# Kernel optimization log

Measured on AMD Instinct MI355X. Metric: run time of the kernel, lower is better.

The kernel has to match this reference:

```python
import jax, jax.numpy as jnp
import numpy as np

N_NODES = 50000
N_EDGES = 800000
IN_DIM = 256
EMB_DIM = 256
N_COMS = 4
D_COM = EMB_DIM // N_COMS  # 64
BN_EPS = 1e-5


def setup_inputs() -> dict:
    key = jax.random.key(0)
    ks = jax.random.split(key, 16)
    s1 = 1.0 / np.sqrt(IN_DIM)
    s2 = 1.0 / np.sqrt(D_COM)
    return {
        "x": jax.random.normal(ks[0], (N_NODES, IN_DIM), jnp.float32),
        "edge_index": jax.random.randint(ks[1], (2, N_EDGES), 0, N_NODES, jnp.int32),
        "ew": jax.random.uniform(ks[2], (N_COMS, N_EDGES), jnp.float32),
        "W1_0": jax.random.normal(ks[3], (N_COMS, IN_DIM, D_COM), jnp.float32) * s1,
        "b1_0": jnp.zeros((N_COMS, D_COM), jnp.float32),
        "W2_0": jax.random.normal(ks[4], (N_COMS, D_COM, D_COM), jnp.float32) * s2,
        "b2_0": jnp.zeros((N_COMS, D_COM), jnp.float32),
        "g0": jnp.ones((N_COMS, D_COM), jnp.float32),
        "bt0": jnp.zeros((N_COMS, D_COM), jnp.float32),
        "W1_1": jax.random.normal(ks[5], (N_COMS, D_COM, D_COM), jnp.float32) * s2,
        "b1_1": jnp.zeros((N_COMS, D_COM), jnp.float32),
        "W2_1": jax.random.normal(ks[6], (N_COMS, D_COM, D_COM), jnp.float32) * s2,
        "b2_1": jnp.zeros((N_COMS, D_COM), jnp.float32),
        "g1": jnp.ones((N_COMS, D_COM), jnp.float32),
        "bt1": jnp.zeros((N_COMS, D_COM), jnp.float32),
        "encW": jax.random.normal(ks[7], (IN_DIM, EMB_DIM), jnp.float32) * s1,
        "encb": jnp.zeros((EMB_DIM,), jnp.float32),
    }


def _gin_bn_relu(h, src, dst, w, W1, b1, W2, b2, gamma, beta):
    # weighted scatter-add aggregation: agg[i] = sum_{e:(j->i)} w_e * h[j]
    msg = h[src] * w[:, None]                       # [E, F]
    agg = jax.ops.segment_sum(msg, dst, num_segments=N_NODES)
    z = h + agg                                      # eps = 0 (train_eps=False)
    z = jax.nn.relu(z @ W1 + b1) @ W2 + b2           # GIN MLP
    mu = jnp.mean(z, axis=0)
    var = jnp.var(z, axis=0)
    z = gamma * (z - mu) * jax.lax.rsqrt(var + BN_EPS) + beta
    return jax.nn.relu(z)                            # dropout: eval mode no-op


def reference(x, edge_index, ew, W1_0, b1_0, W2_0, b2_0, g0, bt0,
              W1_1, b1_1, W2_1, b2_1, g1, bt1, encW, encb):
    src, dst = edge_index[0], edge_index[1]
    outs1, outs2 = [], []
    for k in range(N_COMS):
        h1 = _gin_bn_relu(x, src, dst, ew[k], W1_0[k], b1_0[k], W2_0[k], b2_0[k], g0[k], bt0[k])
        h2 = _gin_bn_relu(h1, src, dst, ew[k], W1_1[k], b1_1[k], W2_1[k], b2_1[k], g1[k], bt1[k])
        outs1.append(h1)
        outs2.append(h2)
    out1 = jnp.concatenate(outs1, axis=-1)  # [N, emb_dim]
    out2 = jnp.concatenate(outs2, axis=-1)  # [N, emb_dim]
    enc = x @ encW + encb                   # input_encoder
    return (enc, out1, out2)
```

## Files before the change

kernel.cpp:

```cpp
#include <hip/hip_runtime.h>

#define NN 50000
#define NE 800000
#define FDIM 256
#define SCAN_BLOCKS 196
#define MMG 782
#define G32 1563

typedef __attribute__((ext_vector_type(8))) short short8v;
typedef __attribute__((ext_vector_type(4))) float float4v;

__device__ __forceinline__ unsigned short f2bf(float f) {
  unsigned u = __float_as_uint(f);
  unsigned r = (u + 0x7fffu + ((u >> 16) & 1u)) >> 16;
  return (unsigned short)r;
}
__device__ __forceinline__ float bf2f(unsigned short b) {
  return __uint_as_float(((unsigned)b) << 16);
}


__global__ __launch_bounds__(256) void k_hist(const int* __restrict__ dst, int* __restrict__ deg16,
                                              int* __restrict__ rank) {
  int e = blockIdx.x * 256 + threadIdx.x;
  if (e < NE) rank[e] = atomicAdd(&deg16[dst[e] << 4], 1);
}

__device__ __forceinline__ int block_incl_scan(int v, int* wsum) {
  const int tid = threadIdx.x;
  const int lane = tid & 63;
  const int w = tid >> 6;
  int incl = v;
  #pragma unroll
  for (int off = 1; off < 64; off <<= 1) {
    int tmp = __shfl_up(incl, off, 64);
    if (lane >= off) incl += tmp;
  }
  if (lane == 63) wsum[w] = incl;
  __syncthreads();
  int woff = 0;
  #pragma unroll
  for (int k = 0; k < 3; k++)
    if (k < w) woff += wsum[k];
  return woff + incl;
}

__global__ __launch_bounds__(256) void k_scan_a(const int* __restrict__ deg16, int* __restrict__ partial) {
  __shared__ int wsum[4];
  int i = blockIdx.x * 256 + threadIdx.x;
  int v = (i < NN) ? deg16[i << 4] : 0;
  int incl = block_incl_scan(v, wsum);
  if (threadIdx.x == 255) partial[blockIdx.x] = incl;
}

__global__ __launch_bounds__(256) void k_scanb_wprep(int* __restrict__ partial, int* __restrict__ offs,
                                                     const float* __restrict__ W1_0, const float* __restrict__ encW,
                                                     const float* __restrict__ W1_1, const float* __restrict__ W2_0,
                                                     const float* __restrict__ W2_1, unsigned short* __restrict__ Bt1,
                                                     unsigned short* __restrict__ BtE, unsigned short* __restrict__ Wb11,
                                                     unsigned short* __restrict__ Wb20, unsigned short* __restrict__ Wb21) {
  if (blockIdx.x == 256) {
    __shared__ int wsum[4];
    int tid = threadIdx.x;
    int v = (tid < SCAN_BLOCKS) ? partial[tid] : 0;
    int incl = block_incl_scan(v, wsum);
    if (tid < SCAN_BLOCKS) partial[tid] = incl - v;
    if (tid == 255) offs[NN] = incl;
    return;
  }
  const int t = blockIdx.x;
  const int k = threadIdx.x;
  const int c = t >> 6, j = t & 63;
  Bt1[t * 256 + k] = f2bf(W1_0[c * 16384 + k * 64 + j]);
  BtE[t * 256 + k] = f2bf(encW[k * 256 + t]);
  if (k < 64) {
    Wb11[c * 4096 + j * 64 + k] = f2bf(W1_1[c * 4096 + k * 64 + j]);
    Wb20[c * 4096 + j * 64 + k] = f2bf(W2_0[c * 4096 + k * 64 + j]);
    Wb21[c * 4096 + j * 64 + k] = f2bf(W2_1[c * 4096 + k * 64 + j]);
  }
}

__global__ __launch_bounds__(256) void k_scan_c(const int* __restrict__ deg16, const int* __restrict__ partial,
                                                int* __restrict__ offs) {
  __shared__ int wsum[4];
  int i = blockIdx.x * 256 + threadIdx.x;
  int v = (i < NN) ? deg16[i << 4] : 0;
  int incl = block_incl_scan(v, wsum);
  int excl = partial[blockIdx.x] + incl - v;
  if (i < NN) offs[i] = excl;
}

__global__ __launch_bounds__(256) void k_fill_mm(const float* __restrict__ x,
                                                 const unsigned short* __restrict__ Bt1,
                                                 const unsigned short* __restrict__ BtE,
                                                 const float* __restrict__ encb,
                                                 const int* __restrict__ srcA, const int* __restrict__ dstA,
                                                 const float* __restrict__ ew, const int* __restrict__ rank,
                                                 const int* __restrict__ offs,
                                                 int4* __restrict__ recs,
                                                 unsigned short* __restrict__ Pout,
                                                 float* __restrict__ encout) {
  __shared__ __align__(16) unsigned short xs[32][264];
  const int tid = threadIdx.x;
  const int lane = tid & 63;
  const int w = tid >> 6;
  const int isE = blockIdx.y;
  const int colw = w * 64;
  const int row0 = blockIdx.x * 32;
  const int lr = lane & 15;
  const int lk = (lane >> 4) * 8;
  const int rbase = (lane >> 4) * 4;

  const int e = (isE * G32 + blockIdx.x) * 256 + tid;
  const bool ev = e < NE;
  const int ec = ev ? e : 0;
  int sA = srcA[ec];
  int dA = dstA[ec];
  int rk = rank[ec];
  float w0 = ew[ec], w1 = ew[NE + ec], w2 = ew[2 * NE + ec], w3 = ew[3 * NE + ec];
  int ob = offs[dA];

  const unsigned short* Bt = isE ? BtE : Bt1;
  const unsigned short* Bptr[4];
  #pragma unroll
  for (int ct = 0; ct < 4; ct++) Bptr[ct] = Bt + (size_t)(colw + ct * 16 + lr) * 256 + lk;

  short8v bcur[4];
  #pragma unroll
  for (int ct = 0; ct < 4; ct++) bcur[ct] = *reinterpret_cast<const short8v*>(Bptr[ct]);

  float4 xv[8];
  #pragma unroll
  for (int it = 0; it < 8; it++) {
    int idx = it * 256 + tid;
    int grow = row0 + (idx >> 6);
    if (grow >= NN) grow = NN - 1;
    xv[it] = *reinterpret_cast<const float4*>(x + (size_t)grow * 256 + (idx & 63) * 4);
  }
  #pragma unroll
  for (int it = 0; it < 8; it++) {
    int idx = it * 256 + tid;
    ushort4 o;
    o.x = f2bf(xv[it].x); o.y = f2bf(xv[it].y); o.z = f2bf(xv[it].z); o.w = f2bf(xv[it].w);
    *reinterpret_cast<ushort4*>(&xs[idx >> 6][(idx & 63) * 4]) = o;
  }

  if (ev) {
    unsigned p01 = (unsigned)f2bf(w0) | ((unsigned)f2bf(w1) << 16);
    unsigned p23 = (unsigned)f2bf(w2) | ((unsigned)f2bf(w3) << 16);
    recs[ob + rk] = make_int4(sA, (int)p01, (int)p23, 0);
  }
  __syncthreads();

  float4v acc[2][4];
  #pragma unroll
  for (int rt = 0; rt < 2; rt++)
    #pragma unroll
    for (int ct = 0; ct < 4; ct++) acc[rt][ct] = (float4v){0.f, 0.f, 0.f, 0.f};

  #pragma unroll
  for (int ks8 = 0; ks8 < 8; ks8++) {
    const int ks = ks8 * 32;
    short8v bnxt[4];
    if (ks8 < 7) {
      #pragma unroll
      for (int ct = 0; ct < 4; ct++) bnxt[ct] = *reinterpret_cast<const short8v*>(Bptr[ct] + ks + 32);
    }
    short8v a[2];
    #pragma unroll
    for (int rt = 0; rt < 2; rt++)
      a[rt] = *reinterpret_cast<const short8v*>(&xs[rt * 16 + lr][ks + lk]);
    #pragma unroll
    for (int rt = 0; rt < 2; rt++)
      #pragma unroll
      for (int ct = 0; ct < 4; ct++)
        acc[rt][ct] = __builtin_amdgcn_mfma_f32_16x16x32_bf16(a[rt], bcur[ct], acc[rt][ct], 0, 0, 0);
    if (ks8 < 7) {
      #pragma unroll
      for (int ct = 0; ct < 4; ct++) bcur[ct] = bnxt[ct];
    }
  }

  __syncthreads();
  if (!isE) {
    #pragma unroll
    for (int rt = 0; rt < 2; rt++)
      #pragma unroll
      for (int ct = 0; ct < 4; ct++) {
        const int col = colw + ct * 16 + lr;
        #pragma unroll
        for (int r = 0; r < 4; r++) xs[rt * 16 + rbase + r][col] = f2bf(acc[rt][ct][r]);
      }
    __syncthreads();
    #pragma unroll
    for (int it = 0; it < 4; it++) {
      int idx = it * 256 + tid;
      int row = idx >> 5;
      int p = idx & 31;
      if (row0 + row < NN)
        *reinterpret_cast<short8v*>(Pout + (size_t)(row0 + row) * 256 + p * 8) =
            *reinterpret_cast<const short8v*>(&xs[row][p * 8]);
    }
  } else {
    float bv[4];
    #pragma unroll
    for (int ct = 0; ct < 4; ct++) bv[ct] = encb[colw + ct * 16 + lr];
    float (*cs)[132] = reinterpret_cast<float(*)[132]>(&xs[0][0]);
    #pragma unroll
    for (int ph = 0; ph < 2; ph++) {
      if ((colw >> 7) == ph) {
        #pragma unroll
        for (int rt = 0; rt < 2; rt++)
          #pragma unroll
          for (int ct = 0; ct < 4; ct++) {
            const int col = colw + ct * 16 + lr - ph * 128;
            #pragma unroll
            for (int r = 0; r < 4; r++) cs[rt * 16 + rbase + r][col] = acc[rt][ct][r] + bv[ct];
          }
      }
      __syncthreads();
      #pragma unroll
      for (int it = 0; it < 4; it++) {
        int idx = it * 256 + tid;
        int row = idx >> 5;
        int p = idx & 31;
        if (row0 + row < NN)
          *reinterpret_cast<float4*>(encout + (size_t)(row0 + row) * 256 + ph * 128 + p * 4) =
              *reinterpret_cast<const float4*>(&cs[row][p * 4]);
      }
      __syncthreads();
    }
  }
}

__global__ __launch_bounds__(256) void k_agg(const unsigned short* __restrict__ P,
                                             const int* __restrict__ offs, const int4* __restrict__ recs,
                                             const float* __restrict__ b1, unsigned short* __restrict__ Rb) {
  const int lane = threadIdx.x & 63;
  const int wid = threadIdx.x >> 6;
  const int i = blockIdx.x * 4 + wid;
  const int half = lane >> 5;
  const int l32 = lane & 31;
  const int col0 = l32 * 8;
  const int c = l32 >> 3;

  const int es = offs[i], ee = offs[i + 1];
  float acc[8];
  #pragma unroll
  for (int j = 0; j < 8; j++) acc[j] = 0.f;

  for (int base = es; base < ee; base += 16) {
    int sq[8];
    float wq[8];
    #pragma unroll
    for (int q = 0; q < 8; q++) {
      int e = base + 2 * q + half;
      bool valid = e < ee;
      int4 rv = recs[valid ? e : es];
      sq[q] = rv.x;
      unsigned p = (c < 2) ? (unsigned)rv.y : (unsigned)rv.z;
      unsigned short wb = (c & 1) ? (unsigned short)(p >> 16) : (unsigned short)(p & 0xffff);
      wq[q] = valid ? bf2f(wb) : 0.f;
    }
    short8v pq[8];
    #pragma unroll
    for (int q = 0; q < 8; q++)
      pq[q] = *reinterpret_cast<const short8v*>(P + (size_t)sq[q] * 256 + col0);
    #pragma unroll
    for (int q = 0; q < 8; q++)
      #pragma unroll
      for (int j = 0; j < 8; j++)
        acc[j] = fmaf(wq[q], bf2f((unsigned short)pq[q][j]), acc[j]);
  }

  #pragma unroll
  for (int j = 0; j < 8; j++) acc[j] += __shfl_xor(acc[j], 32);

  if (half == 0) {
    short8v ps = *reinterpret_cast<const short8v*>(P + (size_t)i * 256 + col0);
    float4 b4a = *reinterpret_cast<const float4*>(b1 + col0);
    float4 b4b = *reinterpret_cast<const float4*>(b1 + col0 + 4);
    float bb[8] = {b4a.x, b4a.y, b4a.z, b4a.w, b4b.x, b4b.y, b4b.z, b4b.w};
    short8v out;
    #pragma unroll
    for (int j = 0; j < 8; j++) {
      float r = bf2f((unsigned short)ps[j]) + acc[j] + bb[j];
      out[j] = (short)f2bf(r > 0.f ? r : 0.f);
    }
    *reinterpret_cast<short8v*>(Rb + (size_t)i * 256 + col0) = out;
  }
}

__global__ __launch_bounds__(256) void k_bd_stats(const unsigned short* __restrict__ A,
                                                  const unsigned short* __restrict__ Wz,
                                                  float* __restrict__ bnsum, float* __restrict__ bnsq) {
  const int lane = threadIdx.x & 63;
  const int c = threadIdx.x >> 6;
  const int row0 = blockIdx.x * 64;
  const int lr = lane & 15;
  const int lk = (lane >> 4) * 8;

  const unsigned short* Aptr[4];
  #pragma unroll
  for (int rt = 0; rt < 4; rt++) {
    int row = row0 + rt * 16 + lr;
    if (row >= NN) row = NN - 1;
    Aptr[rt] = A + (size_t)row * 256 + c * 64 + lk;
  }

  float4v acc[4][4];
  #pragma unroll
  for (int rt = 0; rt < 4; rt++)
    #pragma unroll
    for (int ct = 0; ct < 4; ct++) acc[rt][ct] = (float4v){0.f, 0.f, 0.f, 0.f};

  #pragma unroll
  for (int ks = 0; ks < 64; ks += 32) {
    short8v a[4], b[4];
    #pragma unroll
    for (int rt = 0; rt < 4; rt++) a[rt] = *reinterpret_cast<const short8v*>(Aptr[rt] + ks);
    #pragma unroll
    for (int ct = 0; ct < 4; ct++)
      b[ct] = *reinterpret_cast<const short8v*>(Wz + (size_t)c * 4096 + (ct * 16 + lr) * 64 + ks + lk);
    #pragma unroll
    for (int rt = 0; rt < 4; rt++)
      #pragma unroll
      for (int ct = 0; ct < 4; ct++)
        acc[rt][ct] = __builtin_amdgcn_mfma_f32_16x16x32_bf16(a[rt], b[ct], acc[rt][ct], 0, 0, 0);
  }

  #pragma unroll
  for (int ct = 0; ct < 4; ct++) {
    const int col = c * 64 + ct * 16 + lr;
    float s1 = 0.f, s2 = 0.f;
    #pragma unroll
    for (int rt = 0; rt < 4; rt++) {
      #pragma unroll
      for (int r = 0; r < 4; r++) {
        const int row = row0 + rt * 16 + (lane >> 4) * 4 + r;
        if (row < NN) {
          float v = acc[rt][ct][r];
          s1 += v;
          s2 += v * v;
        }
      }
    }
    s1 += __shfl_xor(s1, 16); s1 += __shfl_xor(s1, 32);
    s2 += __shfl_xor(s2, 16); s2 += __shfl_xor(s2, 32);
    if (lane < 16) {
      atomicAdd(&bnsum[col], s1);
      atomicAdd(&bnsq[col], s2);
    }
  }
}

template <int WITH_P2>
__global__ __launch_bounds__(256) void k_bd_bn(const unsigned short* __restrict__ A,
                                               const unsigned short* __restrict__ Wz,
                                               const float* __restrict__ bnsum, const float* __restrict__ bnsq,
                                               const float* __restrict__ g, const float* __restrict__ bt,
                                               const unsigned short* __restrict__ Wp,
                                               float* __restrict__ Hout, unsigned short* __restrict__ P2out) {
  __shared__ __align__(16) unsigned short h_lds[64][264];
  const int lane = threadIdx.x & 63;
  const int c = threadIdx.x >> 6;
  const int row0 = blockIdx.x * 64;
  const int lr = lane & 15;
  const int lk = (lane >> 4) * 8;
  const int rbase = (lane >> 4) * 4;

  const unsigned short* Aptr[4];
  #pragma unroll
  for (int rt = 0; rt < 4; rt++) {
    int row = row0 + rt * 16 + lr;
    if (row >= NN) row = NN - 1;
    Aptr[rt] = A + (size_t)row * 256 + c * 64 + lk;
  }

  float4v acc[4][4];
  #pragma unroll
  for (int rt = 0; rt < 4; rt++)
    #pragma unroll
    for (int ct = 0; ct < 4; ct++) acc[rt][ct] = (float4v){0.f, 0.f, 0.f, 0.f};

  #pragma unroll
  for (int ks = 0; ks < 64; ks += 32) {
    short8v a[4], b[4];
    #pragma unroll
    for (int rt = 0; rt < 4; rt++) a[rt] = *reinterpret_cast<const short8v*>(Aptr[rt] + ks);
    #pragma unroll
    for (int ct = 0; ct < 4; ct++)
      b[ct] = *reinterpret_cast<const short8v*>(Wz + (size_t)c * 4096 + (ct * 16 + lr) * 64 + ks + lk);
    #pragma unroll
    for (int rt = 0; rt < 4; rt++)
      #pragma unroll
      for (int ct = 0; ct < 4; ct++)
        acc[rt][ct] = __builtin_amdgcn_mfma_f32_16x16x32_bf16(a[rt], b[ct], acc[rt][ct], 0, 0, 0);
  }

  float sc[4], sh[4];
  #pragma unroll
  for (int ct = 0; ct < 4; ct++) {
    const int t = c * 64 + ct * 16 + lr;
    float mu = bnsum[t] * (1.f / NN);
    float var = bnsq[t] * (1.f / NN) - mu * mu;
    var = var > 0.f ? var : 0.f;
    float rs = rsqrtf(var + 1e-5f);
    sc[ct] = g[t] * rs;
    sh[ct] = bt[t] - mu * sc[ct];
  }

  #pragma unroll
  for (int rt = 0; rt < 4; rt++) {
    #pragma unroll
    for (int ct = 0; ct < 4; ct++) {
      const int col = c * 64 + ct * 16 + lr;
      #pragma unroll
      for (int r = 0; r < 4; r++) {
        const int rowl = rt * 16 + rbase + r;
        const int row = row0 + rowl;
        float h = fmaf(acc[rt][ct][r], sc[ct], sh[ct]);
        h = h > 0.f ? h : 0.f;
        if (row < NN) Hout[(size_t)row * 256 + col] = h;
        if (WITH_P2) h_lds[rowl][col] = f2bf(h);
      }
    }
  }

  if (WITH_P2) {
    __syncthreads();
    float4v acc2[4][4];
    #pragma unroll
    for (int rt = 0; rt < 4; rt++)
      #pragma unroll
      for (int ct = 0; ct < 4; ct++) acc2[rt][ct] = (float4v){0.f, 0.f, 0.f, 0.f};
    #pragma unroll
    for (int ks = 0; ks < 64; ks += 32) {
      short8v a[4], b[4];
      #pragma unroll
      for (int rt = 0; rt < 4; rt++)
        a[rt] = *reinterpret_cast<const short8v*>(&h_lds[rt * 16 + lr][c * 64 + ks + lk]);
      #pragma unroll
      for (int ct = 0; ct < 4; ct++)
        b[ct] = *reinterpret_cast<const short8v*>(Wp + (size_t)c * 4096 + (ct * 16 + lr) * 64 + ks + lk);
      #pragma unroll
      for (int rt = 0; rt < 4; rt++)
        #pragma unroll
        for (int ct = 0; ct < 4; ct++)
          acc2[rt][ct] = __builtin_amdgcn_mfma_f32_16x16x32_bf16(a[rt], b[ct], acc2[rt][ct], 0, 0, 0);
    }
    #pragma unroll
    for (int rt = 0; rt < 4; rt++) {
      #pragma unroll
      for (int ct = 0; ct < 4; ct++) {
        const int col = c * 64 + ct * 16 + lr;
        #pragma unroll
        for (int r = 0; r < 4; r++) {
          const int row = row0 + rt * 16 + rbase + r;
          if (row < NN) P2out[(size_t)row * 256 + col] = f2bf(acc2[rt][ct][r]);
        }
      }
    }
  }
}


extern "C" void kernel_launch(void* const* d_in, const int* in_sizes, int n_in,
                              void* d_out, int out_size, void* d_ws, size_t ws_size,
                              hipStream_t stream) {
  const float* x    = (const float*)d_in[0];
  const int*   ei   = (const int*)d_in[1];
  const float* ew   = (const float*)d_in[2];
  const float* W1_0 = (const float*)d_in[3];
  const float* b1_0 = (const float*)d_in[4];
  const float* W2_0 = (const float*)d_in[5];
  const float* g0   = (const float*)d_in[7];
  const float* bt0  = (const float*)d_in[8];
  const float* W1_1 = (const float*)d_in[9];
  const float* b1_1 = (const float*)d_in[10];
  const float* W2_1 = (const float*)d_in[11];
  const float* g1   = (const float*)d_in[13];
  const float* bt1  = (const float*)d_in[14];
  const float* encW = (const float*)d_in[15];
  const float* encb = (const float*)d_in[16];

  const int* srcA = ei;
  const int* dstA = ei + NE;

  float* out_enc = (float*)d_out;
  float* out1 = out_enc + (size_t)NN * FDIM;
  float* out2 = out1 + (size_t)NN * FDIM;

  unsigned short* P1bf = (unsigned short*)out1;
  unsigned short* P2bf = (unsigned short*)out2;

  char* wp = (char*)d_ws;
  auto carve = [&](size_t bytes) {
    char* r = wp;
    wp += (bytes + 255) & ~(size_t)255;
    return r;
  };
  int*   deg16   = (int*)carve((size_t)NN * 16 * 4);
  float* bnsum0  = (float*)carve(256 * 4);
  float* bnsq0   = (float*)carve(256 * 4);
  float* bnsum1  = (float*)carve(256 * 4);
  float* bnsq1   = (float*)carve(256 * 4);
  int*   offs    = (int*)carve((size_t)(NN + 1) * 4);
  int*   rank    = (int*)carve((size_t)NE * 4);
  int*   partial = (int*)carve(SCAN_BLOCKS * 4);
  unsigned short* Bt1  = (unsigned short*)carve(256 * 256 * 2);
  unsigned short* BtE  = (unsigned short*)carve(256 * 256 * 2);
  unsigned short* Wb11 = (unsigned short*)carve(4 * 64 * 64 * 2);
  unsigned short* Wb20 = (unsigned short*)carve(4 * 64 * 64 * 2);
  unsigned short* Wb21 = (unsigned short*)carve(4 * 64 * 64 * 2);
  int4* recs           = (int4*)carve((size_t)NE * 16);
  unsigned short* Rb   = (unsigned short*)carve((size_t)NN * FDIM * 2);

  const size_t zspan = (((size_t)NN * 16 * 4 + 255) & ~(size_t)255) + 4 * 1024;
  hipMemsetAsync(deg16, 0, zspan, stream);

  k_hist<<<(NE + 255) / 256, 256, 0, stream>>>(dstA, deg16, rank);
  k_scan_a<<<SCAN_BLOCKS, 256, 0, stream>>>(deg16, partial);
  k_scanb_wprep<<<257, 256, 0, stream>>>(partial, offs, W1_0, encW, W1_1, W2_0, W2_1,
                                         Bt1, BtE, Wb11, Wb20, Wb21);
  k_scan_c<<<SCAN_BLOCKS, 256, 0, stream>>>(deg16, partial, offs);

  k_fill_mm<<<dim3(G32, 2), 256, 0, stream>>>(x, Bt1, BtE, encb, srcA, dstA, ew, rank, offs,
                                              recs, P1bf, out_enc);

  k_agg<<<NN / 4, 256, 0, stream>>>(P1bf, offs, recs, b1_0, Rb);
  k_bd_stats<<<MMG, 256, 0, stream>>>(Rb, Wb20, bnsum0, bnsq0);
  k_bd_bn<1><<<MMG, 256, 0, stream>>>(Rb, Wb20, bnsum0, bnsq0, g0, bt0, Wb11, out1, P2bf);

  k_agg<<<NN / 4, 256, 0, stream>>>(P2bf, offs, recs, b1_1, Rb);
  k_bd_stats<<<MMG, 256, 0, stream>>>(Rb, Wb21, bnsum1, bnsq1);
  k_bd_bn<0><<<MMG, 256, 0, stream>>>(Rb, Wb21, bnsum1, bnsq1, g1, bt1, nullptr, out2, nullptr);
}
```

Before: 345.6 us.

## Compute P1 and encoder GEMMs in one block sharing the staged x tile

The fused fill+GEMM kernel used to launch two grid slices, each loading and converting the same 32-row x tile to bf16, one for the W1_0 projection and one for the encoder. Now a single block loads x once and runs both MFMA accumulations, writing P1 in bf16 and enc in fp32, and each thread handles two edge records instead of one. This halves the global reads and bf16 conversion of x. The price is twice the accumulator registers and the loss of B-fragment prefetching, which may lower occupancy and expose load latency.

```diff
diff --git a/kernel.cpp b/kernel.cpp
--- a/kernel.cpp
+++ b/kernel.cpp
@@ -104,30 +104,31 @@
   const int tid = threadIdx.x;
   const int lane = tid & 63;
   const int w = tid >> 6;
-  const int isE = blockIdx.y;
   const int colw = w * 64;
   const int row0 = blockIdx.x * 32;
   const int lr = lane & 15;
   const int lk = (lane >> 4) * 8;
   const int rbase = (lane >> 4) * 4;
 
-  const int e = (isE * G32 + blockIdx.x) * 256 + tid;
-  const bool ev = e < NE;
-  const int ec = ev ? e : 0;
-  int sA = srcA[ec];
-  int dA = dstA[ec];
-  int rk = rank[ec];
-  float w0 = ew[ec], w1 = ew[NE + ec], w2 = ew[2 * NE + ec], w3 = ew[3 * NE + ec];
-  int ob = offs[dA];
-
-  const unsigned short* Bt = isE ? BtE : Bt1;
-  const unsigned short* Bptr[4];
-  #pragma unroll
-  for (int ct = 0; ct < 4; ct++) Bptr[ct] = Bt + (size_t)(colw + ct * 16 + lr) * 256 + lk;
-
-  short8v bcur[4];
-  #pragma unroll
-  for (int ct = 0; ct < 4; ct++) bcur[ct] = *reinterpret_cast<const short8v*>(Bptr[ct]);
+  const int e0 = blockIdx.x * 512 + tid * 2;
+  int sA[2], dA[2], rk[2], ob[2];
+  float w0[2], w1[2], w2[2], w3[2];
+  bool ev[2];
+  #pragma unroll
+  for (int q = 0; q < 2; q++) {
+    int e = e0 + q;
+    ev[q] = e < NE;
+    int ec = ev[q] ? e : 0;
+    sA[q] = srcA[ec];
+    dA[q] = dstA[ec];
+    rk[q] = rank[ec];
+    w0[q] = ew[ec];
+    w1[q] = ew[NE + ec];
+    w2[q] = ew[2 * NE + ec];
+    w3[q] = ew[3 * NE + ec];
+  }
+  #pragma unroll
+  for (int q = 0; q < 2; q++) ob[q] = offs[dA[q]];
 
   float4 xv[8];
   #pragma unroll
@@ -145,26 +146,41 @@
     *reinterpret_cast<ushort4*>(&xs[idx >> 6][(idx & 63) * 4]) = o;
   }
 
-  if (ev) {
-    unsigned p01 = (unsigned)f2bf(w0) | ((unsigned)f2bf(w1) << 16);
-    unsigned p23 = (unsigned)f2bf(w2) | ((unsigned)f2bf(w3) << 16);
-    recs[ob + rk] = make_int4(sA, (int)p01, (int)p23, 0);
+  #pragma unroll
+  for (int q = 0; q < 2; q++) {
+    if (ev[q]) {
+      unsigned p01 = (unsigned)f2bf(w0[q]) | ((unsigned)f2bf(w1[q]) << 16);
+      unsigned p23 = (unsigned)f2bf(w2[q]) | ((unsigned)f2bf(w3[q]) << 16);
+      recs[ob[q] + rk[q]] = make_int4(sA[q], (int)p01, (int)p23, 0);
+    }
   }
   __syncthreads();
 
-  float4v acc[2][4];
+  float4v aP[2][4], aE[2][4];
   #pragma unroll
   for (int rt = 0; rt < 2; rt++)
     #pragma unroll
-    for (int ct = 0; ct < 4; ct++) acc[rt][ct] = (float4v){0.f, 0.f, 0.f, 0.f};
+    for (int ct = 0; ct < 4; ct++) {
+      aP[rt][ct] = (float4v){0.f, 0.f, 0.f, 0.f};
+      aE[rt][ct] = (float4v){0.f, 0.f, 0.f, 0.f};
+    }
+
+  const unsigned short* BptrP[4];
+  const unsigned short* BptrE[4];
+  #pragma unroll
+  for (int ct = 0; ct < 4; ct++) {
+    BptrP[ct] = Bt1 + (size_t)(colw + ct * 16 + lr) * 256 + lk;
+    BptrE[ct] = BtE + (size_t)(colw + ct * 16 + lr) * 256 + lk;
+  }
 
   #pragma unroll
   for (int ks8 = 0; ks8 < 8; ks8++) {
     const int ks = ks8 * 32;
-    short8v bnxt[4];
-    if (ks8 < 7) {
-      #pragma unroll
-      for (int ct = 0; ct < 4; ct++) bnxt[ct] = *reinterpret_cast<const short8v*>(Bptr[ct] + ks + 32);
+    short8v bP[4], bE[4];
+    #pragma unroll
+    for (int ct = 0; ct < 4; ct++) {
+      bP[ct] = *reinterpret_cast<const short8v*>(BptrP[ct] + ks);
+      bE[ct] = *reinterpret_cast<const short8v*>(BptrE[ct] + ks);
     }
     short8v a[2];
     #pragma unroll
@@ -173,24 +189,48 @@
     #pragma unroll
     for (int rt = 0; rt < 2; rt++)
       #pragma unroll
-      for (int ct = 0; ct < 4; ct++)
-        acc[rt][ct] = __builtin_amdgcn_mfma_f32_16x16x32_bf16(a[rt], bcur[ct], acc[rt][ct], 0, 0, 0);
-    if (ks8 < 7) {
-      #pragma unroll
-      for (int ct = 0; ct < 4; ct++) bcur[ct] = bnxt[ct];
-    }
+      for (int ct = 0; ct < 4; ct++) {
+        aP[rt][ct] = __builtin_amdgcn_mfma_f32_16x16x32_bf16(a[rt], bP[ct], aP[rt][ct], 0, 0, 0);
+        aE[rt][ct] = __builtin_amdgcn_mfma_f32_16x16x32_bf16(a[rt], bE[ct], aE[rt][ct], 0, 0, 0);
+      }
   }
 
   __syncthreads();
-  if (!isE) {
-    #pragma unroll
-    for (int rt = 0; rt < 2; rt++)
-      #pragma unroll
-      for (int ct = 0; ct < 4; ct++) {
-        const int col = colw + ct * 16 + lr;
+  #pragma unroll
+  for (int rt = 0; rt < 2; rt++)
+    #pragma unroll
+    for (int ct = 0; ct < 4; ct++) {
+      const int col = colw + ct * 16 + lr;
+      #pragma unroll
+      for (int r = 0; r < 4; r++) xs[rt * 16 + rbase + r][col] = f2bf(aP[rt][ct][r]);
+    }
+  __syncthreads();
+  #pragma unroll
+  for (int it = 0; it < 4; it++) {
+    int idx = it * 256 + tid;
+    int row = idx >> 5;
+    int p = idx & 31;
+    if (row0 + row < NN)
+      *reinterpret_cast<short8v*>(Pout + (size_t)(row0 + row) * 256 + p * 8) =
+          *reinterpret_cast<const short8v*>(&xs[row][p * 8]);
+  }
+  __syncthreads();
+  float bv[4];
+  #pragma unroll
+  for (int ct = 0; ct < 4; ct++) bv[ct] = encb[colw + ct * 16 + lr];
+  float (*cs)[132] = reinterpret_cast<float(*)[132]>(&xs[0][0]);
+  #pragma unroll
+  for (int ph = 0; ph < 2; ph++) {
+    if ((colw >> 7) == ph) {
+      #pragma unroll
+      for (int rt = 0; rt < 2; rt++)
         #pragma unroll
-        for (int r = 0; r < 4; r++) xs[rt * 16 + rbase + r][col] = f2bf(acc[rt][ct][r]);
-      }
+        for (int ct = 0; ct < 4; ct++) {
+          const int col = colw + ct * 16 + lr - ph * 128;
+          #pragma unroll
+          for (int r = 0; r < 4; r++) cs[rt * 16 + rbase + r][col] = aE[rt][ct][r] + bv[ct];
+        }
+    }
     __syncthreads();
     #pragma unroll
     for (int it = 0; it < 4; it++) {
@@ -198,38 +238,10 @@
       int row = idx >> 5;
       int p = idx & 31;
       if (row0 + row < NN)
-        *reinterpret_cast<short8v*>(Pout + (size_t)(row0 + row) * 256 + p * 8) =
-            *reinterpret_cast<const short8v*>(&xs[row][p * 8]);
-    }
-  } else {
-    float bv[4];
-    #pragma unroll
-    for (int ct = 0; ct < 4; ct++) bv[ct] = encb[colw + ct * 16 + lr];
-    float (*cs)[132] = reinterpret_cast<float(*)[132]>(&xs[0][0]);
-    #pragma unroll
-    for (int ph = 0; ph < 2; ph++) {
-      if ((colw >> 7) == ph) {
-        #pragma unroll
-        for (int rt = 0; rt < 2; rt++)
-          #pragma unroll
-          for (int ct = 0; ct < 4; ct++) {
-            const int col = colw + ct * 16 + lr - ph * 128;
-            #pragma unroll
-            for (int r = 0; r < 4; r++) cs[rt * 16 + rbase + r][col] = acc[rt][ct][r] + bv[ct];
-          }
-      }
-      __syncthreads();
-      #pragma unroll
-      for (int it = 0; it < 4; it++) {
-        int idx = it * 256 + tid;
-        int row = idx >> 5;
-        int p = idx & 31;
-        if (row0 + row < NN)
-          *reinterpret_cast<float4*>(encout + (size_t)(row0 + row) * 256 + ph * 128 + p * 4) =
-              *reinterpret_cast<const float4*>(&cs[row][p * 4]);
-      }
-      __syncthreads();
-    }
+        *reinterpret_cast<float4*>(encout + (size_t)(row0 + row) * 256 + ph * 128 + p * 4) =
+            *reinterpret_cast<const float4*>(&cs[row][p * 4]);
+    }
+    __syncthreads();
   }
 }
 
@@ -525,8 +537,8 @@
                                          Bt1, BtE, Wb11, Wb20, Wb21);
   k_scan_c<<<SCAN_BLOCKS, 256, 0, stream>>>(deg16, partial, offs);
 
-  k_fill_mm<<<dim3(G32, 2), 256, 0, stream>>>(x, Bt1, BtE, encb, srcA, dstA, ew, rank, offs,
-                                              recs, P1bf, out_enc);
+  k_fill_mm<<<G32, 256, 0, stream>>>(x, Bt1, BtE, encb, srcA, dstA, ew, rank, offs,
+                                     recs, P1bf, out_enc);
 
   k_agg<<<NN / 4, 256, 0, stream>>>(P1bf, offs, recs, b1_0, Rb);
   k_bd_stats<<<MMG, 256, 0, stream>>>(Rb, Wb20, bnsum0, bnsq0);
```

Result: no change. 349.6 us (+1.1%).
